# Optimization experiments

Measured on AMD Instinct MI355X. Metric: run time of the kernel, lower is better.

Reference implementation:

```python
import jax, jax.numpy as jnp
import numpy as np

N = 20000        # nodes
E = 320000       # edges (before self-loops)
G = 128          # graphs
NODE_DIM = 128
H = 256
L = 4
EPS = 1e-5


def setup_inputs() -> dict:
    key = jax.random.key(0)
    ks = jax.random.split(key, 12)
    x = jax.random.normal(ks[0], (N, NODE_DIM), jnp.float32)
    edge_index = jax.random.randint(ks[1], (2, E), 0, N, dtype=jnp.int32)
    batch = jnp.sort(jax.random.randint(ks[2], (N,), 0, G, dtype=jnp.int32))
    s_in = 1.0 / np.sqrt(NODE_DIM)
    s_h = 1.0 / np.sqrt(H)
    return {
        "x": x,
        "edge_index": edge_index,
        "batch": batch,
        "enc_w": jax.random.normal(ks[3], (NODE_DIM, H), jnp.float32) * s_in,
        "enc_b": jnp.zeros((H,), jnp.float32),
        "conv_w": jax.random.normal(ks[4], (L, H, H), jnp.float32) * s_h,
        "conv_b": jnp.zeros((L, H), jnp.float32),
        "bn_gamma": jnp.ones((L, H), jnp.float32),
        "bn_beta": jnp.zeros((L, H), jnp.float32),
        "bn_mean": jnp.zeros((L, H), jnp.float32),
        "bn_var": jnp.ones((L, H), jnp.float32),
        "head_w1": jax.random.normal(ks[5], (2 * H, H), jnp.float32) * (1.0 / np.sqrt(2 * H)),
        "head_b1": jnp.zeros((H,), jnp.float32),
        "head_w2": jax.random.normal(ks[6], (H, 1), jnp.float32) * s_h,
        "head_b2": jnp.zeros((1,), jnp.float32),
    }


def reference(x, edge_index, batch, enc_w, enc_b, conv_w, conv_b,
              bn_gamma, bn_beta, bn_mean, bn_var,
              head_w1, head_b1, head_w2, head_b2):
    seg = jax.ops.segment_sum
    # GCN normalization with added self-loops (PyG GCNConv default)
    loops = jnp.arange(N, dtype=edge_index.dtype)
    src = jnp.concatenate([edge_index[0], loops])
    dst = jnp.concatenate([edge_index[1], loops])
    deg = seg(jnp.ones(src.shape[0], x.dtype), dst, num_segments=N)  # >= 1
    dinv = jax.lax.rsqrt(deg)
    norm = dinv[src] * dinv[dst]  # [E+N]

    h = x @ enc_w + enc_b  # [N, H]
    for l in range(L):
        m = h @ conv_w[l]                                    # transform
        m = seg(m[src] * norm[:, None], dst, num_segments=N)  # gather-norm-scatter
        m = m + conv_b[l]
        m = jax.nn.relu(m)
        # BatchNorm1d (eval mode: running stats); dropout inactive in eval
        m = (m - bn_mean[l]) * jax.lax.rsqrt(bn_var[l] + EPS) * bn_gamma[l] + bn_beta[l]
        h = h + m  # residual

    # global mean + add pooling over graphs
    sums = seg(h, batch, num_segments=G)                     # [G, H]
    counts = seg(jnp.ones((N,), h.dtype), batch, num_segments=G)
    mean = sums / jnp.maximum(counts, 1.0)[:, None]
    g = jnp.concatenate([mean, sums], axis=-1)               # [G, 2H]

    out = jax.nn.relu(g @ head_w1 + head_b1) @ head_w2 + head_b2
    return out.squeeze(-1)  # [G]
```

## Files before the change

kernel.cpp:

```cpp
#include <hip/hip_runtime.h>

#define N_NODES 20000
#define N_EDGES 320000
#define N_GRAPHS 128
#define IN_DIM 128
#define HDIM 256
#define LAYERS 4
#define EPSV 1e-5f
#define PCH 16
#define ELLS 64
#define NBLK_AGG (N_NODES / 4)

#define XQ (N_NODES * IN_DIM / 4)
#define ENC_N (HDIM * IN_DIM)
#define CONV_N (LAYERS * HDIM * HDIM)
#define BN_N (LAYERS * HDIM)
#define PREP_TOTAL (XQ + ENC_N + CONV_N + BN_N + N_NODES)

typedef unsigned short u16;
typedef __attribute__((ext_vector_type(8))) __bf16 bf16x8;
typedef __attribute__((ext_vector_type(4))) float f32x4;
typedef __attribute__((ext_vector_type(8))) unsigned short u16x8;

__device__ __forceinline__ u16 f2bf(float f) {
    unsigned int u = __float_as_uint(f);
    u += 0x7FFFu + ((u >> 16) & 1u);
    return (u16)(u >> 16);
}
__device__ __forceinline__ float bf2f(u16 s) {
    return __uint_as_float((unsigned int)s << 16);
}

__global__ __launch_bounds__(256) void k_prep(
    const float* __restrict__ x, u16* __restrict__ xb,
    const float* __restrict__ enc_w, u16* __restrict__ encT,
    const float* __restrict__ conv_w, u16* __restrict__ convT,
    const float* __restrict__ gamma, const float* __restrict__ beta,
    const float* __restrict__ mean, const float* __restrict__ var,
    float* __restrict__ bnA, float* __restrict__ bnB, int* __restrict__ cnt)
{
    int idx = blockIdx.x * 256 + threadIdx.x;
    if (idx < XQ) {
        float4 v = *reinterpret_cast<const float4*>(x + (size_t)idx * 4);
        ushort4 o;
        o.x = f2bf(v.x); o.y = f2bf(v.y); o.z = f2bf(v.z); o.w = f2bf(v.w);
        *reinterpret_cast<ushort4*>(xb + (size_t)idx * 4) = o;
        return;
    }
    idx -= XQ;
    if (idx < ENC_N) {
        int n = idx / IN_DIM, k = idx - n * IN_DIM;
        encT[idx] = f2bf(enc_w[(size_t)k * HDIM + n]);
        return;
    }
    idx -= ENC_N;
    if (idx < CONV_N) {
        int l = idx >> 16, i = idx & 65535;
        int n = i >> 8, k = i & 255;
        convT[idx] = f2bf(conv_w[((size_t)l << 16) + (size_t)k * HDIM + n]);
        return;
    }
    idx -= CONV_N;
    if (idx < BN_N) {
        float A = gamma[idx] * rsqrtf(var[idx] + EPSV);
        bnA[idx] = A;
        bnB[idx] = beta[idx] - mean[idx] * A;
        return;
    }
    idx -= BN_N;
    if (idx < N_NODES) cnt[idx] = 0;
}

__global__ void k_scatter_ell(const int* __restrict__ src, const int* __restrict__ dst,
                              int* __restrict__ cnt, int* __restrict__ col) {
    int e = blockIdx.x * 256 + threadIdx.x;
    if (e < N_EDGES) {
        int d = dst[e];
        int s = src[e];
        int p = atomicAdd(&cnt[d], 1);
        if (p < ELLS) col[(size_t)d * ELLS + p] = s;
    }
}

__device__ __forceinline__ bf16x8 load_frag(const u16* __restrict__ lds, int r, int g) {
    const char* rb = (const char*)(lds + r * 32);
    int s = (r & 3) << 4;
    union { struct { unsigned long long lo, hi; } q; bf16x8 v; } u;
    u.q.lo = *(const unsigned long long*)(rb + ((g * 8) ^ s));
    u.q.hi = *(const unsigned long long*)(rb + ((32 + g * 8) ^ s));
    return u.v;
}

template <int K, int MODE>
__global__ __launch_bounds__(256) void k_gemm_mfma(
    const u16* __restrict__ A, const u16* __restrict__ BT,
    const float* __restrict__ bias, u16* __restrict__ Cb, int M)
{
    constexpr int NT = K / 32;
    __shared__ u16 As[2][128 * 32];
    __shared__ u16 Bs[2][128 * 32];
    const int tid = threadIdx.x;
    const int lane = tid & 63;
    const int wv = tid >> 6, wr = wv >> 1, wc = wv & 1;
    const int m0 = blockIdx.x * 128, n0 = blockIdx.y * 128;
    const int g = lane >> 4, lr = lane & 15;

    f32x4 acc[4][4] = {};

    auto stage = [&](int buf, int k0) {
        #pragma unroll
        for (int j = 0; j < 2; j++) {
            int q = tid + 256 * j;
            int r = q >> 2, c4 = q & 3;
            int boff = (c4 * 16) ^ ((r & 3) << 4);
            int arow = m0 + r; if (arow >= M) arow = M - 1;
            const char* ga = (const char*)(A + (size_t)arow * K + k0) + boff;
            const char* gb = (const char*)(BT + (size_t)(n0 + r) * K + k0) + boff;
            __builtin_amdgcn_global_load_lds(
                (const __attribute__((address_space(1))) void*)ga,
                (__attribute__((address_space(3))) void*)((char*)As[buf] + q * 16), 16, 0, 0);
            __builtin_amdgcn_global_load_lds(
                (const __attribute__((address_space(1))) void*)gb,
                (__attribute__((address_space(3))) void*)((char*)Bs[buf] + q * 16), 16, 0, 0);
        }
    };

    stage(0, 0);
    #pragma unroll
    for (int kt = 0; kt < NT; kt++) {
        const int cur = kt & 1;
        if (kt + 1 < NT) {
            stage(cur ^ 1, (kt + 1) * 32);
            asm volatile("s_waitcnt vmcnt(4)" ::: "memory");
        } else {
            asm volatile("s_waitcnt vmcnt(0)" ::: "memory");
        }
        __builtin_amdgcn_sched_barrier(0);
        __builtin_amdgcn_s_barrier();
        __builtin_amdgcn_sched_barrier(0);

        bf16x8 af[4], bfr[4];
        #pragma unroll
        for (int mi = 0; mi < 4; mi++) af[mi] = load_frag(As[cur], wr * 64 + mi * 16 + lr, g);
        #pragma unroll
        for (int ni = 0; ni < 4; ni++) bfr[ni] = load_frag(Bs[cur], wc * 64 + ni * 16 + lr, g);
        #pragma unroll
        for (int mi = 0; mi < 4; mi++)
            #pragma unroll
            for (int ni = 0; ni < 4; ni++)
                acc[mi][ni] = __builtin_amdgcn_mfma_f32_16x16x32_bf16(
                    af[mi], bfr[ni], acc[mi][ni], 0, 0, 0);

        asm volatile("s_waitcnt lgkmcnt(0)" ::: "memory");
        __builtin_amdgcn_sched_barrier(0);
        __builtin_amdgcn_s_barrier();
        __builtin_amdgcn_sched_barrier(0);
    }

    #pragma unroll
    for (int mi = 0; mi < 4; mi++) {
        #pragma unroll
        for (int rg = 0; rg < 4; rg++) {
            int row = m0 + wr * 64 + mi * 16 + g * 4 + rg;
            if (row >= M) continue;
            #pragma unroll
            for (int ni = 0; ni < 4; ni++) {
                int colg = n0 + wc * 64 + ni * 16 + lr;
                float v = acc[mi][ni][rg];
                if (MODE == 0) v += bias[colg];
                Cb[(size_t)row * HDIM + colg] = f2bf(v);
            }
        }
    }
}

template <int WRITEH>
__global__ __launch_bounds__(256) void k_aggregate(
    const u16* __restrict__ mb, const int* __restrict__ cnt,
    const int* __restrict__ col,
    const float* __restrict__ cb, const float* __restrict__ bnA,
    const float* __restrict__ bnB,
    float* __restrict__ h, u16* __restrict__ hb)
{
    const int node = blockIdx.x * 4 + (threadIdx.x >> 6);
    const int lane = threadIdx.x & 63;
    const int p = lane >> 5;
    const int c = (lane & 31) * 8;
    int nb = cnt[node]; if (nb > ELLS) nb = ELLS;
    const float di = rsqrtf((float)nb + 1.0f);

    int s_l = 0; float w_l = 0.f;
    if (lane < nb) {
        s_l = col[(size_t)node * ELLS + lane];
        w_l = rsqrtf((float)cnt[s_l] + 1.0f) * di;
    }

    float a[8] = {};
    if (p == 0) {
        float dii = di * di;
        u16x8 v = *reinterpret_cast<const u16x8*>(mb + (size_t)node * HDIM + c);
        #pragma unroll
        for (int j = 0; j < 8; j++) a[j] = dii * bf2f(v[j]);
    }

    const int iters = (nb + 1) >> 1;
    for (int t = 0; t < iters; t += 8) {
        int e = 2 * t + p;
        int   s0 = __shfl(s_l, e,      64); float w0 = __shfl(w_l, e,      64);
        int   s1 = __shfl(s_l, e + 2,  64); float w1 = __shfl(w_l, e + 2,  64);
        int   s2 = __shfl(s_l, e + 4,  64); float w2 = __shfl(w_l, e + 4,  64);
        int   s3 = __shfl(s_l, e + 6,  64); float w3 = __shfl(w_l, e + 6,  64);
        int   s4 = __shfl(s_l, e + 8,  64); float w4 = __shfl(w_l, e + 8,  64);
        int   s5 = __shfl(s_l, e + 10, 64); float w5 = __shfl(w_l, e + 10, 64);
        int   s6 = __shfl(s_l, e + 12, 64); float w6 = __shfl(w_l, e + 12, 64);
        int   s7 = __shfl(s_l, e + 14, 64); float w7 = __shfl(w_l, e + 14, 64);
        u16x8 v0 = *reinterpret_cast<const u16x8*>(mb + (size_t)s0 * HDIM + c);
        u16x8 v1 = *reinterpret_cast<const u16x8*>(mb + (size_t)s1 * HDIM + c);
        u16x8 v2 = *reinterpret_cast<const u16x8*>(mb + (size_t)s2 * HDIM + c);
        u16x8 v3 = *reinterpret_cast<const u16x8*>(mb + (size_t)s3 * HDIM + c);
        u16x8 v4 = *reinterpret_cast<const u16x8*>(mb + (size_t)s4 * HDIM + c);
        u16x8 v5 = *reinterpret_cast<const u16x8*>(mb + (size_t)s5 * HDIM + c);
        u16x8 v6 = *reinterpret_cast<const u16x8*>(mb + (size_t)s6 * HDIM + c);
        u16x8 v7 = *reinterpret_cast<const u16x8*>(mb + (size_t)s7 * HDIM + c);
        #pragma unroll
        for (int j = 0; j < 8; j++) {
            a[j] += w0 * bf2f(v0[j]) + w1 * bf2f(v1[j]);
            a[j] += w2 * bf2f(v2[j]) + w3 * bf2f(v3[j]);
            a[j] += w4 * bf2f(v4[j]) + w5 * bf2f(v5[j]);
            a[j] += w6 * bf2f(v6[j]) + w7 * bf2f(v7[j]);
        }
    }

    #pragma unroll
    for (int j = 0; j < 8; j++) a[j] += __shfl_xor(a[j], 32, 64);

    if (p == 0) {
        const size_t base = (size_t)node * HDIM + c;
        u16x8 rv = *reinterpret_cast<const u16x8*>(hb + base);
        float4 cb0 = *reinterpret_cast<const float4*>(cb + c);
        float4 cb1 = *reinterpret_cast<const float4*>(cb + c + 4);
        float4 A0 = *reinterpret_cast<const float4*>(bnA + c);
        float4 A1 = *reinterpret_cast<const float4*>(bnA + c + 4);
        float4 B0 = *reinterpret_cast<const float4*>(bnB + c);
        float4 B1 = *reinterpret_cast<const float4*>(bnB + c + 4);
        float cbv[8] = {cb0.x, cb0.y, cb0.z, cb0.w, cb1.x, cb1.y, cb1.z, cb1.w};
        float Av[8] = {A0.x, A0.y, A0.z, A0.w, A1.x, A1.y, A1.z, A1.w};
        float Bv[8] = {B0.x, B0.y, B0.z, B0.w, B1.x, B1.y, B1.z, B1.w};
        float hn[8];
        #pragma unroll
        for (int j = 0; j < 8; j++) {
            float v = fmaxf(a[j] + cbv[j], 0.f);
            hn[j] = bf2f(rv[j]) + v * Av[j] + Bv[j];
        }
        if (WRITEH) {
            float4 o0, o1;
            o0.x = hn[0]; o0.y = hn[1]; o0.z = hn[2]; o0.w = hn[3];
            o1.x = hn[4]; o1.y = hn[5]; o1.z = hn[6]; o1.w = hn[7];
            *reinterpret_cast<float4*>(h + base) = o0;
            *reinterpret_cast<float4*>(h + base + 4) = o1;
        } else {
            u16x8 hbv;
            #pragma unroll
            for (int j = 0; j < 8; j++) hbv[j] = f2bf(hn[j]);
            *reinterpret_cast<u16x8*>(hb + base) = hbv;
        }
    }
}

__device__ __forceinline__ int lower_bound_dev(const int* a, int n, int key) {
    int lo = 0, hi = n;
    while (lo < hi) {
        int mid = (lo + hi) >> 1;
        if (a[mid] < key) lo = mid + 1; else hi = mid;
    }
    return lo;
}

__global__ __launch_bounds__(256) void k_pool_partial(const float* __restrict__ h,
                                                      const int* __restrict__ batch,
                                                      float* __restrict__ pbuf) {
    int g = blockIdx.x / PCH, c = blockIdx.x % PCH;
    int t = threadIdx.x;
    int start = lower_bound_dev(batch, N_NODES, g);
    int end = lower_bound_dev(batch, N_NODES, g + 1);
    int len = end - start;
    int s0 = start + (int)(((long long)len * c) / PCH);
    int s1 = start + (int)(((long long)len * (c + 1)) / PCH);
    float acc = 0.f;
    for (int n = s0; n < s1; n++) acc += h[(size_t)n * HDIM + t];
    pbuf[(size_t)blockIdx.x * HDIM + t] = acc;
}

__global__ __launch_bounds__(256) void k_head(const float* __restrict__ pbuf,
                                              const int* __restrict__ batch,
                                              const float* __restrict__ w1,
                                              const float* __restrict__ b1,
                                              const float* __restrict__ w2,
                                              const float* __restrict__ b2,
                                              float* __restrict__ out) {
    int g = blockIdx.x;
    int t = threadIdx.x;
    __shared__ float gs[512];
    __shared__ float red[256];
    float s = 0.f;
    #pragma unroll
    for (int c = 0; c < PCH; c++) s += pbuf[(size_t)(g * PCH + c) * HDIM + t];
    int start = lower_bound_dev(batch, N_NODES, g);
    int end = lower_bound_dev(batch, N_NODES, g + 1);
    float cntf = fmaxf((float)(end - start), 1.0f);
    gs[t] = s / cntf;
    gs[256 + t] = s;
    __syncthreads();
    float acc = b1[t];
    for (int k = 0; k < 512; k++) acc += gs[k] * w1[(size_t)k * HDIM + t];
    acc = fmaxf(acc, 0.f);
    red[t] = acc * w2[t];
    __syncthreads();
    for (int s2 = 128; s2 > 0; s2 >>= 1) {
        if (t < s2) red[t] += red[t + s2];
        __syncthreads();
    }
    if (t == 0) out[g] = red[0] + b2[0];
}

extern "C" void kernel_launch(void* const* d_in, const int* in_sizes, int n_in,
                              void* d_out, int out_size, void* d_ws, size_t ws_size,
                              hipStream_t stream) {
    const float* x      = (const float*)d_in[0];
    const int*   ei     = (const int*)d_in[1];
    const int*   srcIdx = ei;
    const int*   dstIdx = ei + N_EDGES;
    const int*   batch  = (const int*)d_in[2];
    const float* enc_w  = (const float*)d_in[3];
    const float* enc_b  = (const float*)d_in[4];
    const float* conv_w = (const float*)d_in[5];
    const float* conv_b = (const float*)d_in[6];
    const float* gamma  = (const float*)d_in[7];
    const float* beta   = (const float*)d_in[8];
    const float* bmean  = (const float*)d_in[9];
    const float* bvar   = (const float*)d_in[10];
    const float* w1     = (const float*)d_in[11];
    const float* b1     = (const float*)d_in[12];
    const float* w2     = (const float*)d_in[13];
    const float* b2     = (const float*)d_in[14];
    float* out = (float*)d_out;

    char* ws = (char*)d_ws;
    size_t off = 0;
    auto alloc = [&](size_t bytes) -> void* {
        void* p = ws + off;
        off = (off + bytes + 255) & ~(size_t)255;
        return p;
    };
    int*   cnt    = (int*)alloc((size_t)N_NODES * 4);
    int*   col    = (int*)alloc((size_t)N_NODES * ELLS * 4);
    float* h      = (float*)alloc((size_t)N_NODES * HDIM * 4);
    u16*   hb     = (u16*)alloc((size_t)N_NODES * HDIM * 2);
    u16*   mb     = (u16*)alloc((size_t)N_NODES * HDIM * 2);
    u16*   encT   = (u16*)alloc((size_t)HDIM * IN_DIM * 2);
    u16*   convT  = (u16*)alloc((size_t)LAYERS * HDIM * HDIM * 2);
    float* bnA    = (float*)alloc((size_t)LAYERS * HDIM * 4);
    float* bnB    = (float*)alloc((size_t)LAYERS * HDIM * 4);
    float* pbuf   = (float*)alloc((size_t)N_GRAPHS * PCH * HDIM * 4);
    u16*   xb     = mb;

    const int nb_edges = (N_EDGES + 255) / 256;

    k_prep<<<(PREP_TOTAL + 255) / 256, 256, 0, stream>>>(
        x, xb, enc_w, encT, conv_w, convT, gamma, beta, bmean, bvar, bnA, bnB, cnt);

    k_scatter_ell<<<nb_edges, 256, 0, stream>>>(srcIdx, dstIdx, cnt, col);

    dim3 gg((N_NODES + 127) / 128, HDIM / 128);
    k_gemm_mfma<IN_DIM, 0><<<gg, 256, 0, stream>>>(xb, encT, enc_b, hb, N_NODES);

    for (int l = 0; l < LAYERS; l++) {
        k_gemm_mfma<HDIM, 1><<<gg, 256, 0, stream>>>(
            hb, convT + (size_t)l * HDIM * HDIM, nullptr, mb, N_NODES);
        if (l < LAYERS - 1)
            k_aggregate<0><<<NBLK_AGG, 256, 0, stream>>>(
                mb, cnt, col,
                conv_b + (size_t)l * HDIM, bnA + (size_t)l * HDIM, bnB + (size_t)l * HDIM,
                h, hb);
        else
            k_aggregate<1><<<NBLK_AGG, 256, 0, stream>>>(
                mb, cnt, col,
                conv_b + (size_t)l * HDIM, bnA + (size_t)l * HDIM, bnB + (size_t)l * HDIM,
                h, hb);
    }

    k_pool_partial<<<N_GRAPHS * PCH, 256, 0, stream>>>(h, batch, pbuf);
    k_head<<<N_GRAPHS, 256, 0, stream>>>(pbuf, batch, w1, b1, w2, b2, out);
}
```

Baseline: 243.4 us.

## Retile GEMM to 128x64 with K=64 stages; keep final hidden state in bf16

The MFMA GEMM tile changes from 128x128 with 32-wide K steps to 128x64 with 64-wide K steps. Each wave now owns 32 rows across all 64 columns, and the grid has twice as many blocks in N. Separately, the last aggregation writes bf16 hb instead of an fp32 h buffer, and pooling reads bf16. This cuts final-layer write and pool read traffic and raises block count for better occupancy. The cost is lower precision in the pooled sums and more total A-matrix reloads.

```diff
diff --git a/kernel.cpp b/kernel.cpp
--- a/kernel.cpp
+++ b/kernel.cpp
@@ -96,42 +96,52 @@
     const u16* __restrict__ A, const u16* __restrict__ BT,
     const float* __restrict__ bias, u16* __restrict__ Cb, int M)
 {
-    constexpr int NT = K / 32;
-    __shared__ u16 As[2][128 * 32];
-    __shared__ u16 Bs[2][128 * 32];
+    constexpr int NT2 = K / 64;
+    __shared__ u16 As[2][2][128 * 32];
+    __shared__ u16 Bs[2][2][64 * 32];
     const int tid = threadIdx.x;
     const int lane = tid & 63;
-    const int wv = tid >> 6, wr = wv >> 1, wc = wv & 1;
-    const int m0 = blockIdx.x * 128, n0 = blockIdx.y * 128;
+    const int wr = tid >> 6;
+    const int m0 = blockIdx.x * 128, n0 = blockIdx.y * 64;
     const int g = lane >> 4, lr = lane & 15;
 
-    f32x4 acc[4][4] = {};
+    f32x4 acc[2][4] = {};
 
     auto stage = [&](int buf, int k0) {
         #pragma unroll
-        for (int j = 0; j < 2; j++) {
-            int q = tid + 256 * j;
-            int r = q >> 2, c4 = q & 3;
-            int boff = (c4 * 16) ^ ((r & 3) << 4);
-            int arow = m0 + r; if (arow >= M) arow = M - 1;
-            const char* ga = (const char*)(A + (size_t)arow * K + k0) + boff;
-            const char* gb = (const char*)(BT + (size_t)(n0 + r) * K + k0) + boff;
-            __builtin_amdgcn_global_load_lds(
-                (const __attribute__((address_space(1))) void*)ga,
-                (__attribute__((address_space(3))) void*)((char*)As[buf] + q * 16), 16, 0, 0);
-            __builtin_amdgcn_global_load_lds(
-                (const __attribute__((address_space(1))) void*)gb,
-                (__attribute__((address_space(3))) void*)((char*)Bs[buf] + q * 16), 16, 0, 0);
+        for (int kk = 0; kk < 2; kk++) {
+            #pragma unroll
+            for (int j = 0; j < 2; j++) {
+                int q = tid + 256 * j;
+                int r = q >> 2, c4 = q & 3;
+                int boff = (c4 * 16) ^ ((r & 3) << 4);
+                int arow = m0 + r; if (arow >= M) arow = M - 1;
+                const char* ga = (const char*)(A + (size_t)arow * K + k0 + kk * 32) + boff;
+                __builtin_amdgcn_global_load_lds(
+                    (const __attribute__((address_space(1))) void*)ga,
+                    (__attribute__((address_space(3))) void*)((char*)As[buf][kk] + q * 16),
+                    16, 0, 0);
+            }
+            {
+                int q = tid;
+                int r = q >> 2, c4 = q & 3;
+                int boff = (c4 * 16) ^ ((r & 3) << 4);
+                const char* gb = (const char*)(BT + (size_t)(n0 + r) * K + k0 + kk * 32) + boff;
+                __builtin_amdgcn_global_load_lds(
+                    (const __attribute__((address_space(1))) void*)gb,
+                    (__attribute__((address_space(3))) void*)((char*)Bs[buf][kk] + q * 16),
+                    16, 0, 0);
+            }
         }
     };
 
     stage(0, 0);
     #pragma unroll
-    for (int kt = 0; kt < NT; kt++) {
+    for (int kt = 0; kt < NT2; kt++) {
         const int cur = kt & 1;
-        if (kt + 1 < NT) {
-            stage(cur ^ 1, (kt + 1) * 32);
-            asm volatile("s_waitcnt vmcnt(4)" ::: "memory");
+        if (kt + 1 < NT2) {
+            stage(cur ^ 1, (kt + 1) * 64);
+            asm volatile("s_waitcnt vmcnt(6)" ::: "memory");
         } else {
             asm volatile("s_waitcnt vmcnt(0)" ::: "memory");
         }
@@ -139,17 +149,22 @@
         __builtin_amdgcn_s_barrier();
         __builtin_amdgcn_sched_barrier(0);
 
-        bf16x8 af[4], bfr[4];
-        #pragma unroll
-        for (int mi = 0; mi < 4; mi++) af[mi] = load_frag(As[cur], wr * 64 + mi * 16 + lr, g);
-        #pragma unroll
-        for (int ni = 0; ni < 4; ni++) bfr[ni] = load_frag(Bs[cur], wc * 64 + ni * 16 + lr, g);
-        #pragma unroll
-        for (int mi = 0; mi < 4; mi++)
+        #pragma unroll
+        for (int kk = 0; kk < 2; kk++) {
+            bf16x8 af[2], bfr[4];
+            #pragma unroll
+            for (int mi = 0; mi < 2; mi++)
+                af[mi] = load_frag(As[cur][kk], wr * 32 + mi * 16 + lr, g);
             #pragma unroll
             for (int ni = 0; ni < 4; ni++)
-                acc[mi][ni] = __builtin_amdgcn_mfma_f32_16x16x32_bf16(
-                    af[mi], bfr[ni], acc[mi][ni], 0, 0, 0);
+                bfr[ni] = load_frag(Bs[cur][kk], ni * 16 + lr, g);
+            #pragma unroll
+            for (int mi = 0; mi < 2; mi++)
+                #pragma unroll
+                for (int ni = 0; ni < 4; ni++)
+                    acc[mi][ni] = __builtin_amdgcn_mfma_f32_16x16x32_bf16(
+                        af[mi], bfr[ni], acc[mi][ni], 0, 0, 0);
+        }
 
         asm volatile("s_waitcnt lgkmcnt(0)" ::: "memory");
         __builtin_amdgcn_sched_barrier(0);
@@ -158,14 +173,14 @@
     }
 
     #pragma unroll
-    for (int mi = 0; mi < 4; mi++) {
+    for (int mi = 0; mi < 2; mi++) {
         #pragma unroll
         for (int rg = 0; rg < 4; rg++) {
-            int row = m0 + wr * 64 + mi * 16 + g * 4 + rg;
+            int row = m0 + wr * 32 + mi * 16 + g * 4 + rg;
             if (row >= M) continue;
             #pragma unroll
             for (int ni = 0; ni < 4; ni++) {
-                int colg = n0 + wc * 64 + ni * 16 + lr;
+                int colg = n0 + ni * 16 + lr;
                 float v = acc[mi][ni][rg];
                 if (MODE == 0) v += bias[colg];
                 Cb[(size_t)row * HDIM + colg] = f2bf(v);
@@ -174,13 +189,11 @@
     }
 }
 
-template <int WRITEH>
 __global__ __launch_bounds__(256) void k_aggregate(
     const u16* __restrict__ mb, const int* __restrict__ cnt,
     const int* __restrict__ col,
     const float* __restrict__ cb, const float* __restrict__ bnA,
-    const float* __restrict__ bnB,
-    float* __restrict__ h, u16* __restrict__ hb)
+    const float* __restrict__ bnB, u16* __restrict__ hb)
 {
     const int node = blockIdx.x * 4 + (threadIdx.x >> 6);
     const int lane = threadIdx.x & 63;
@@ -246,24 +259,13 @@
         float cbv[8] = {cb0.x, cb0.y, cb0.z, cb0.w, cb1.x, cb1.y, cb1.z, cb1.w};
         float Av[8] = {A0.x, A0.y, A0.z, A0.w, A1.x, A1.y, A1.z, A1.w};
         float Bv[8] = {B0.x, B0.y, B0.z, B0.w, B1.x, B1.y, B1.z, B1.w};
-        float hn[8];
+        u16x8 hbv;
         #pragma unroll
         for (int j = 0; j < 8; j++) {
             float v = fmaxf(a[j] + cbv[j], 0.f);
-            hn[j] = bf2f(rv[j]) + v * Av[j] + Bv[j];
-        }
-        if (WRITEH) {
-            float4 o0, o1;
-            o0.x = hn[0]; o0.y = hn[1]; o0.z = hn[2]; o0.w = hn[3];
-            o1.x = hn[4]; o1.y = hn[5]; o1.z = hn[6]; o1.w = hn[7];
-            *reinterpret_cast<float4*>(h + base) = o0;
-            *reinterpret_cast<float4*>(h + base + 4) = o1;
-        } else {
-            u16x8 hbv;
-            #pragma unroll
-            for (int j = 0; j < 8; j++) hbv[j] = f2bf(hn[j]);
-            *reinterpret_cast<u16x8*>(hb + base) = hbv;
-        }
+            hbv[j] = f2bf(bf2f(rv[j]) + v * Av[j] + Bv[j]);
+        }
+        *reinterpret_cast<u16x8*>(hb + base) = hbv;
     }
 }
 
@@ -276,7 +278,7 @@
     return lo;
 }
 
-__global__ __launch_bounds__(256) void k_pool_partial(const float* __restrict__ h,
+__global__ __launch_bounds__(256) void k_pool_partial(const u16* __restrict__ hb,
                                                       const int* __restrict__ batch,
                                                       float* __restrict__ pbuf) {
     int g = blockIdx.x / PCH, c = blockIdx.x % PCH;
@@ -287,7 +289,7 @@
     int s0 = start + (int)(((long long)len * c) / PCH);
     int s1 = start + (int)(((long long)len * (c + 1)) / PCH);
     float acc = 0.f;
-    for (int n = s0; n < s1; n++) acc += h[(size_t)n * HDIM + t];
+    for (int n = s0; n < s1; n++) acc += bf2f(hb[(size_t)n * HDIM + t]);
     pbuf[(size_t)blockIdx.x * HDIM + t] = acc;
 }
 
@@ -354,7 +356,6 @@
     };
     int*   cnt    = (int*)alloc((size_t)N_NODES * 4);
     int*   col    = (int*)alloc((size_t)N_NODES * ELLS * 4);
-    float* h      = (float*)alloc((size_t)N_NODES * HDIM * 4);
     u16*   hb     = (u16*)alloc((size_t)N_NODES * HDIM * 2);
     u16*   mb     = (u16*)alloc((size_t)N_NODES * HDIM * 2);
     u16*   encT   = (u16*)alloc((size_t)HDIM * IN_DIM * 2);
@@ -371,24 +372,18 @@
 
     k_scatter_ell<<<nb_edges, 256, 0, stream>>>(srcIdx, dstIdx, cnt, col);
 
-    dim3 gg((N_NODES + 127) / 128, HDIM / 128);
+    dim3 gg((N_NODES + 127) / 128, HDIM / 64);
     k_gemm_mfma<IN_DIM, 0><<<gg, 256, 0, stream>>>(xb, encT, enc_b, hb, N_NODES);
 
     for (int l = 0; l < LAYERS; l++) {
         k_gemm_mfma<HDIM, 1><<<gg, 256, 0, stream>>>(
             hb, convT + (size_t)l * HDIM * HDIM, nullptr, mb, N_NODES);
-        if (l < LAYERS - 1)
-            k_aggregate<0><<<NBLK_AGG, 256, 0, stream>>>(
-                mb, cnt, col,
-                conv_b + (size_t)l * HDIM, bnA + (size_t)l * HDIM, bnB + (size_t)l * HDIM,
-                h, hb);
-        else
-            k_aggregate<1><<<NBLK_AGG, 256, 0, stream>>>(
-                mb, cnt, col,
-                conv_b + (size_t)l * HDIM, bnA + (size_t)l * HDIM, bnB + (size_t)l * HDIM,
-                h, hb);
-    }
-
-    k_pool_partial<<<N_GRAPHS * PCH, 256, 0, stream>>>(h, batch, pbuf);
+        k_aggregate<<<NBLK_AGG, 256, 0, stream>>>(
+            mb, cnt, col,
+            conv_b + (size_t)l * HDIM, bnA + (size_t)l * HDIM, bnB + (size_t)l * HDIM,
+            hb);
+    }
+
+    k_pool_partial<<<N_GRAPHS * PCH, 256, 0, stream>>>(hb, batch, pbuf);
     k_head<<<N_GRAPHS, 256, 0, stream>>>(pbuf, batch, w1, b1, w2, b2, out);
 }
```

Measured after the change: 230.5 us. 5.3% less time.
